# Performance work log

Hardware: AMD Instinct MI355X
Metric: run time of the kernel (lower is better)

## Reference

```python
import jax, jax.numpy as jnp
import numpy as np

B, S, H, D, DM = 2, 512, 8, 32, 256  # batch, seq_len, n_head, d_k, d_model


def setup_inputs() -> dict:
    key = jax.random.key(0)
    ks = jax.random.split(key, 8)
    scale = 0.02
    return {
        "hidden_states": jax.random.normal(ks[0], (B, S, DM), dtype=jnp.float32),
        "rpe": jax.random.normal(ks[1], (B, S, S, D), dtype=jnp.float32),
        "w_q": jax.random.normal(ks[2], (DM, H * D), dtype=jnp.float32) * scale,
        "w_k": jax.random.normal(ks[3], (DM, H * D), dtype=jnp.float32) * scale,
        "w_v": jax.random.normal(ks[4], (DM, H * D), dtype=jnp.float32) * scale,
        "fc_w": jax.random.normal(ks[5], (H * D, DM), dtype=jnp.float32) * scale,
        "fc_b": jnp.zeros((DM,), dtype=jnp.float32),
        "ln_w": jnp.ones((DM,), dtype=jnp.float32),
        "ln_b": jnp.zeros((DM,), dtype=jnp.float32),
        "station_num": 256,
    }


def reference(hidden_states, rpe, w_q, w_k, w_v, fc_w, fc_b, ln_w, ln_b, station_num):
    b, s, dm = hidden_states.shape
    d = rpe.shape[-1]
    h = w_q.shape[1] // d

    def heads(x, w):
        # (b, s, dm) @ (dm, h*d) -> (b, h, s, d)
        return (x @ w).reshape(b, s, h, d).transpose(0, 2, 1, 3)

    q = heads(hidden_states, w_q)
    k = heads(hidden_states, w_k)
    v = heads(hidden_states, w_v)

    # torch: (q.unsqueeze(2) * k.unsqueeze(3) * rpe.unsqueeze(1)).sum(-1)
    # scores[b,h,i,j] = sum_d q[b,h,j,d] * k[b,h,i,d] * rpe[b,i,j,d]
    scores = jnp.einsum('bhjd,bhid,bijd->bhij', q, k, rpe) / jnp.sqrt(jnp.float32(d))

    # shielded mask: column j visible if j < station_num, plus the diagonal
    col = jnp.arange(s) < station_num                  # (s,)
    mask = col[None, :] | jnp.eye(s, dtype=bool)        # (s, s)
    scores = jnp.where(mask[None, None], scores, jnp.float32(-1e10))

    attn = jax.nn.softmax(scores, axis=-1)              # (b, h, s, s)
    out = jnp.einsum('bhij,bhjd->bhid', attn, v)        # (b, h, s, d)
    out = out.transpose(0, 2, 1, 3).reshape(b, s, h * d)

    ctx = out @ fc_w + fc_b + hidden_states             # residual
    mu = jnp.mean(ctx, axis=-1, keepdims=True)
    var = jnp.mean(jnp.square(ctx - mu), axis=-1, keepdims=True)
    ctx = (ctx - mu) / jnp.sqrt(var + 1e-6) * ln_w + ln_b
    return ctx
```

## Files before the change

kernel.cpp:

```cpp
#include <hip/hip_runtime.h>
#include <hip/hip_bf16.h>

#define B_  2
#define S_  512
#define H_  8
#define D_  32
#define DM_ 256
#define HD_ 256
#define NROW 4
#define TI  2
#define HC  2
#define NR  (TI * HC)

__global__ __launch_bounds__(256) void qkv_kernel(
    const float* __restrict__ hid, const float* __restrict__ wq,
    const float* __restrict__ wk, const float* __restrict__ wv,
    float* __restrict__ qo, float* __restrict__ ko, float* __restrict__ vo)
{
  __shared__ float hs[NROW][DM_];
  const int r0 = blockIdx.x * NROW;
  const float* w   = (blockIdx.y == 0) ? wq : (blockIdx.y == 1) ? wk : wv;
  float*       out = (blockIdx.y == 0) ? qo : (blockIdx.y == 1) ? ko : vo;
  const float mulf = (blockIdx.y == 0) ? 0.17677669529663687f : 1.0f;
  const int tid = threadIdx.x;

  for (int idx = tid; idx < NROW * DM_; idx += 256)
    hs[idx >> 8][idx & 255] = hid[r0 * DM_ + idx];
  __syncthreads();

  float acc[NROW] = {0.f, 0.f, 0.f, 0.f};
  const float* wp = w + tid;
  #pragma unroll 8
  for (int c4 = 0; c4 < DM_ / 4; ++c4) {
    const float w0 = wp[(4 * c4 + 0) * HD_];
    const float w1 = wp[(4 * c4 + 1) * HD_];
    const float w2 = wp[(4 * c4 + 2) * HD_];
    const float w3 = wp[(4 * c4 + 3) * HD_];
    #pragma unroll
    for (int r = 0; r < NROW; ++r) {
      const float4 hv = reinterpret_cast<const float4*>(&hs[r][0])[c4];
      acc[r] = fmaf(hv.x, w0, acc[r]);
      acc[r] = fmaf(hv.y, w1, acc[r]);
      acc[r] = fmaf(hv.z, w2, acc[r]);
      acc[r] = fmaf(hv.w, w3, acc[r]);
    }
  }
  const int h = tid >> 5, d = tid & 31;
  #pragma unroll
  for (int r = 0; r < NROW; ++r) {
    const int g = r0 + r;
    const int b = g >> 9, s = g & (S_ - 1);
    out[((b * H_ + h) * S_ + s) * D_ + d] = acc[r] * mulf;
  }
}

__device__ __forceinline__ float red4(float x) {
  int i;
  i = __builtin_amdgcn_mov_dpp(__float_as_int(x), 0xB1, 0xf, 0xf, true);
  x += __int_as_float(i);
  i = __builtin_amdgcn_mov_dpp(__float_as_int(x), 0x4E, 0xf, 0xf, true);
  x += __int_as_float(i);
  return x;
}

__global__ __launch_bounds__(256, 4) void attn_kernel(
    const float* __restrict__ rpe, const float* __restrict__ q_ws,
    const float* __restrict__ k_ws, const float* __restrict__ v_ws,
    const int* __restrict__ station_p, float* __restrict__ o_ws)
{
  __shared__ float p_smem[NR * S_];
  __shared__ float sums[NR];

  const int tid  = threadIdx.x;
  const int w    = tid >> 6, lane = tid & 63;
  const int j4   = lane >> 2, dq = lane & 3;
  const int j8   = lane >> 3, dc = lane & 7;
  const int n    = blockIdx.x;
  const int hg   = (n >> 3) & 3;
  const int t    = (n & 7) | ((n >> 5) << 3);
  const int b    = t >> 8;
  const int i0   = (t & 255) * TI;
  const int h0   = hg * HC;
  const int HS   = S_ * D_;

  int station = station_p[0];
  station = station > S_ ? S_ : (station < 0 ? 0 : station);

  const float* qb = q_ws + (size_t)((b * H_ + h0) * S_) * D_;
  const float* kb = k_ws + (size_t)((b * H_ + h0) * S_ + i0) * D_;
  const float* vb = v_ws + (size_t)((b * H_ + h0) * S_) * D_;
  const float* rb = rpe + ((size_t)b * S_ + i0) * S_ * D_;

  float4 kf[HC][TI][2];
  #pragma unroll
  for (int hh = 0; hh < HC; ++hh)
    #pragma unroll
    for (int ii = 0; ii < TI; ++ii) {
      kf[hh][ii][0] = *reinterpret_cast<const float4*>(kb + hh * HS + ii * D_ + dq * 8);
      kf[hh][ii][1] = *reinterpret_cast<const float4*>(kb + hh * HS + ii * D_ + dq * 8 + 4);
    }

  for (int jb = w * 16; jb < station; jb += 64) {
    const int j  = jb + j4;
    const int jc = j < S_ ? j : S_ - 1;
    float4 q[HC][2];
    #pragma unroll
    for (int hh = 0; hh < HC; ++hh) {
      q[hh][0] = *reinterpret_cast<const float4*>(qb + hh * HS + jc * D_ + dq * 8);
      q[hh][1] = *reinterpret_cast<const float4*>(qb + hh * HS + jc * D_ + dq * 8 + 4);
    }
    float4 rv[TI][2];
    #pragma unroll
    for (int ii = 0; ii < TI; ++ii) {
      rv[ii][0] = *reinterpret_cast<const float4*>(rb + ii * HS + jc * D_ + dq * 8);
      rv[ii][1] = *reinterpret_cast<const float4*>(rb + ii * HS + jc * D_ + dq * 8 + 4);
    }
    #pragma unroll
    for (int hh = 0; hh < HC; ++hh)
      #pragma unroll
      for (int ii = 0; ii < TI; ++ii) {
        float s = q[hh][0].x * kf[hh][ii][0].x * rv[ii][0].x;
        s = fmaf(q[hh][0].y * kf[hh][ii][0].y, rv[ii][0].y, s);
        s = fmaf(q[hh][0].z * kf[hh][ii][0].z, rv[ii][0].z, s);
        s = fmaf(q[hh][0].w * kf[hh][ii][0].w, rv[ii][0].w, s);
        s = fmaf(q[hh][1].x * kf[hh][ii][1].x, rv[ii][1].x, s);
        s = fmaf(q[hh][1].y * kf[hh][ii][1].y, rv[ii][1].y, s);
        s = fmaf(q[hh][1].z * kf[hh][ii][1].z, rv[ii][1].z, s);
        s = fmaf(q[hh][1].w * kf[hh][ii][1].w, rv[ii][1].w, s);
        s = red4(s);
        if (dq == 0 && j < station) p_smem[(hh * TI + ii) * S_ + j] = s;
      }
  }
  if (w == 0 && j4 < TI) {
    const int j = i0 + j4;
    if (j >= station) {
      const float4 r0 = *reinterpret_cast<const float4*>(rb + j4 * HS + j * D_ + dq * 8);
      const float4 r1 = *reinterpret_cast<const float4*>(rb + j4 * HS + j * D_ + dq * 8 + 4);
      #pragma unroll
      for (int hh = 0; hh < HC; ++hh) {
        const float4 q0 = *reinterpret_cast<const float4*>(qb + hh * HS + j * D_ + dq * 8);
        const float4 q1 = *reinterpret_cast<const float4*>(qb + hh * HS + j * D_ + dq * 8 + 4);
        const float4 k0 = *reinterpret_cast<const float4*>(kb + hh * HS + j4 * D_ + dq * 8);
        const float4 k1 = *reinterpret_cast<const float4*>(kb + hh * HS + j4 * D_ + dq * 8 + 4);
        float s = q0.x * k0.x * r0.x;
        s = fmaf(q0.y * k0.y, r0.y, s);
        s = fmaf(q0.z * k0.z, r0.z, s);
        s = fmaf(q0.w * k0.w, r0.w, s);
        s = fmaf(q1.x * k1.x, r1.x, s);
        s = fmaf(q1.y * k1.y, r1.y, s);
        s = fmaf(q1.z * k1.z, r1.z, s);
        s = fmaf(q1.w * k1.w, r1.w, s);
        s = red4(s);
        if (dq == 0) p_smem[(hh * TI + j4) * S_ + j] = s;
      }
    }
  }
  __syncthreads();

  {
    const int r  = w;
    const int ii = r & (TI - 1);
    const int ig = i0 + ii;
    const bool dx = (ig >= station);
    float m = -1e30f;
    for (int jj = lane; jj < station; jj += 64) m = fmaxf(m, p_smem[r * S_ + jj]);
    const float dv = dx ? p_smem[r * S_ + ig] : -1e30f;
    m = fmaxf(m, dv);
    #pragma unroll
    for (int o = 32; o; o >>= 1) m = fmaxf(m, __shfl_xor(m, o, 64));
    float sum = 0.f;
    for (int jj = lane; jj < station; jj += 64) {
      const float e = __expf(p_smem[r * S_ + jj] - m);
      p_smem[r * S_ + jj] = e;
      sum += e;
    }
    #pragma unroll
    for (int o = 32; o; o >>= 1) sum += __shfl_xor(sum, o, 64);
    if (dx) {
      const float e = __expf(dv - m);
      sum += e;
      if (lane == 0) p_smem[r * S_ + ig] = e;
    }
    if (lane == 0) sums[r] = sum;
  }
  __syncthreads();

  float4 acc[HC][TI];
  #pragma unroll
  for (int hh = 0; hh < HC; ++hh)
    #pragma unroll
    for (int ii = 0; ii < TI; ++ii) acc[hh][ii] = make_float4(0.f, 0.f, 0.f, 0.f);

  for (int jb = w * 8; jb < station; jb += 32) {
    const int j  = jb + j8;
    const int jc = j < S_ ? j : S_ - 1;
    float4 v4[HC];
    #pragma unroll
    for (int hh = 0; hh < HC; ++hh)
      v4[hh] = *reinterpret_cast<const float4*>(vb + hh * HS + jc * D_ + dc * 4);
    #pragma unroll
    for (int hh = 0; hh < HC; ++hh)
      #pragma unroll
      for (int ii = 0; ii < TI; ++ii) {
        float pv = 0.f;
        if (j < station) pv = p_smem[(hh * TI + ii) * S_ + j];
        acc[hh][ii].x = fmaf(pv, v4[hh].x, acc[hh][ii].x);
        acc[hh][ii].y = fmaf(pv, v4[hh].y, acc[hh][ii].y);
        acc[hh][ii].z = fmaf(pv, v4[hh].z, acc[hh][ii].z);
        acc[hh][ii].w = fmaf(pv, v4[hh].w, acc[hh][ii].w);
      }
  }
  if (w == 0 && j8 == 0) {
    #pragma unroll
    for (int ii = 0; ii < TI; ++ii) {
      const int ig = i0 + ii;
      if (ig >= station) {
        #pragma unroll
        for (int hh = 0; hh < HC; ++hh) {
          const float pv = p_smem[(hh * TI + ii) * S_ + ig];
          const float4 v4 = *reinterpret_cast<const float4*>(vb + hh * HS + ig * D_ + dc * 4);
          acc[hh][ii].x = fmaf(pv, v4.x, acc[hh][ii].x);
          acc[hh][ii].y = fmaf(pv, v4.y, acc[hh][ii].y);
          acc[hh][ii].z = fmaf(pv, v4.z, acc[hh][ii].z);
          acc[hh][ii].w = fmaf(pv, v4.w, acc[hh][ii].w);
        }
      }
    }
  }
  __syncthreads();

  float4* redv = reinterpret_cast<float4*>(p_smem);
  #pragma unroll
  for (int hh = 0; hh < HC; ++hh)
    #pragma unroll
    for (int ii = 0; ii < TI; ++ii) {
      const int r = hh * TI + ii;
      float4 a = acc[hh][ii];
      a.x += __shfl_xor(a.x, 8);
      a.y += __shfl_xor(a.y, 8);
      a.z += __shfl_xor(a.z, 8);
      a.w += __shfl_xor(a.w, 8);
      if ((j8 & 1) == 0)
        redv[((w * 4 + (j8 >> 1)) * NR + r) * 8 + dc] = a;
    }
  __syncthreads();
  if (tid < NR * 8) {
    const int r = tid >> 3, d4 = tid & 7;
    float4 a = make_float4(0.f, 0.f, 0.f, 0.f);
    #pragma unroll
    for (int g = 0; g < 16; ++g) {
      const float4 x = redv[(g * NR + r) * 8 + d4];
      a.x += x.x; a.y += x.y; a.z += x.z; a.w += x.w;
    }
    const float inv = 1.f / sums[r];
    a.x *= inv; a.y *= inv; a.z *= inv; a.w *= inv;
    const int hh = r >> 1, ii = r & 1;
    reinterpret_cast<float4*>(
        o_ws + (size_t)((b * H_ + h0 + hh) * S_ + i0 + ii) * D_)[d4] = a;
  }
}

__global__ __launch_bounds__(256) void fc_ln_kernel(
    const float* __restrict__ o_ws, const float* __restrict__ fc_w,
    const float* __restrict__ fc_b, const float* __restrict__ hid,
    const float* __restrict__ ln_w, const float* __restrict__ ln_b,
    float* __restrict__ out)
{
  __shared__ float orow[NROW][HD_];
  __shared__ float red[NROW][4];
  const int tid = threadIdx.x;
  const int r0 = blockIdx.x * NROW;

  for (int idx = tid; idx < NROW * HD_; idx += 256) {
    const int r = idx >> 8, m = idx & 255;
    const int g = r0 + r;
    const int b = g >> 9, i = g & (S_ - 1);
    orow[r][m] = o_ws[((b * H_ + (m >> 5)) * S_ + i) * D_ + (m & 31)];
  }
  __syncthreads();

  float acc[NROW] = {0.f, 0.f, 0.f, 0.f};
  const float* wp = fc_w + tid;
  #pragma unroll 8
  for (int n4 = 0; n4 < HD_ / 4; ++n4) {
    const float w0 = wp[(4 * n4 + 0) * DM_];
    const float w1 = wp[(4 * n4 + 1) * DM_];
    const float w2 = wp[(4 * n4 + 2) * DM_];
    const float w3 = wp[(4 * n4 + 3) * DM_];
    #pragma unroll
    for (int r = 0; r < NROW; ++r) {
      const float4 ov = reinterpret_cast<const float4*>(&orow[r][0])[n4];
      acc[r] = fmaf(ov.x, w0, acc[r]);
      acc[r] = fmaf(ov.y, w1, acc[r]);
      acc[r] = fmaf(ov.z, w2, acc[r]);
      acc[r] = fmaf(ov.w, w3, acc[r]);
    }
  }
  const float bias = fc_b[tid];
  #pragma unroll
  for (int r = 0; r < NROW; ++r) acc[r] += bias + hid[(r0 + r) * DM_ + tid];

  const int w = tid >> 6, lane = tid & 63;
  float mu[NROW];
  #pragma unroll
  for (int r = 0; r < NROW; ++r) {
    float s = acc[r];
    #pragma unroll
    for (int o = 32; o; o >>= 1) s += __shfl_xor(s, o, 64);
    if (lane == 0) red[r][w] = s;
  }
  __syncthreads();
  #pragma unroll
  for (int r = 0; r < NROW; ++r)
    mu[r] = (red[r][0] + red[r][1] + red[r][2] + red[r][3]) * (1.f / DM_);
  __syncthreads();
  #pragma unroll
  for (int r = 0; r < NROW; ++r) {
    const float dd = acc[r] - mu[r];
    float s = dd * dd;
    #pragma unroll
    for (int o = 32; o; o >>= 1) s += __shfl_xor(s, o, 64);
    if (lane == 0) red[r][w] = s;
  }
  __syncthreads();
  const float lw = ln_w[tid], lb = ln_b[tid];
  #pragma unroll
  for (int r = 0; r < NROW; ++r) {
    const float var = (red[r][0] + red[r][1] + red[r][2] + red[r][3]) * (1.f / DM_);
    out[(r0 + r) * DM_ + tid] =
        (acc[r] - mu[r]) * rsqrtf(var + 1e-6f) * lw + lb;
  }
}

extern "C" void kernel_launch(void* const* d_in, const int* in_sizes, int n_in,
                              void* d_out, int out_size, void* d_ws, size_t ws_size,
                              hipStream_t stream) {
  const float* hid = (const float*)d_in[0];
  const float* rpe = (const float*)d_in[1];
  const float* wq  = (const float*)d_in[2];
  const float* wk  = (const float*)d_in[3];
  const float* wv  = (const float*)d_in[4];
  const float* fcw = (const float*)d_in[5];
  const float* fcb = (const float*)d_in[6];
  const float* lnw = (const float*)d_in[7];
  const float* lnb = (const float*)d_in[8];
  const int* station = (const int*)d_in[9];
  float* out = (float*)d_out;

  const size_t per = (size_t)B_ * H_ * S_ * D_;
  float* q_ws = (float*)d_ws;
  float* k_ws = q_ws + per;
  float* v_ws = k_ws + per;
  float* o_ws = v_ws + per;

  dim3 gA(B_ * S_ / NROW, 3);
  qkv_kernel<<<gA, 256, 0, stream>>>(hid, wq, wk, wv, q_ws, k_ws, v_ws);
  attn_kernel<<<B_ * (S_ / TI) * (H_ / HC), 256, 0, stream>>>(
      rpe, q_ws, k_ws, v_ws, station, o_ws);
  fc_ln_kernel<<<B_ * S_ / NROW, 256, 0, stream>>>(o_ws, fcw, fcb, hid, lnw, lnb, out);
}
```

Before: 156.7 us.

## Stream rpe tiles into double-buffered LDS via global_load_lds DMA

```diff
diff --git a/kernel.cpp b/kernel.cpp
--- a/kernel.cpp
+++ b/kernel.cpp
@@ -11,6 +11,7 @@
 #define TI  2
 #define HC  2
 #define NR  (TI * HC)
+#define JC  32
 
 __global__ __launch_bounds__(256) void qkv_kernel(
     const float* __restrict__ hid, const float* __restrict__ wq,
@@ -54,27 +55,38 @@
   }
 }
 
-__device__ __forceinline__ float red4(float x) {
+__device__ __forceinline__ float red8(float x) {
   int i;
   i = __builtin_amdgcn_mov_dpp(__float_as_int(x), 0xB1, 0xf, 0xf, true);
   x += __int_as_float(i);
   i = __builtin_amdgcn_mov_dpp(__float_as_int(x), 0x4E, 0xf, 0xf, true);
   x += __int_as_float(i);
+  i = __builtin_amdgcn_mov_dpp(__float_as_int(x), 0x124, 0xf, 0xf, true);
+  x += __int_as_float(i);
   return x;
 }
 
-__global__ __launch_bounds__(256, 4) void attn_kernel(
+__device__ __forceinline__ void lds_dma16(float* dst_uniform, const float* src) {
+  __builtin_amdgcn_global_load_lds(
+      (const __attribute__((address_space(1))) unsigned int*)src,
+      (__attribute__((address_space(3))) unsigned int*)dst_uniform,
+      16, 0, 0);
+}
+
+__global__ __launch_bounds__(256, 6) void attn_kernel(
     const float* __restrict__ rpe, const float* __restrict__ q_ws,
     const float* __restrict__ k_ws, const float* __restrict__ v_ws,
     const int* __restrict__ station_p, float* __restrict__ o_ws)
 {
-  __shared__ float p_smem[NR * S_];
+  __shared__ __align__(16) float rpe_smem[2][TI * JC * D_];
+  __shared__ __align__(16) float p_smem[NR * S_];
   __shared__ float sums[NR];
 
   const int tid  = threadIdx.x;
   const int w    = tid >> 6, lane = tid & 63;
-  const int j4   = lane >> 2, dq = lane & 3;
-  const int j8   = lane >> 3, dc = lane & 7;
+  const int jl   = tid >> 3;
+  const int dc   = tid & 7;
+  const int j8   = lane >> 3;
   const int n    = blockIdx.x;
   const int hg   = (n >> 3) & 3;
   const int t    = (n & 7) | ((n >> 5) << 3);
@@ -85,73 +97,100 @@
 
   int station = station_p[0];
   station = station > S_ ? S_ : (station < 0 ? 0 : station);
+  const int NC = (station + JC - 1) / JC;
 
   const float* qb = q_ws + (size_t)((b * H_ + h0) * S_) * D_;
   const float* kb = k_ws + (size_t)((b * H_ + h0) * S_ + i0) * D_;
   const float* vb = v_ws + (size_t)((b * H_ + h0) * S_) * D_;
   const float* rb = rpe + ((size_t)b * S_ + i0) * S_ * D_;
 
-  float4 kf[HC][TI][2];
+  float4 kf[HC][TI];
   #pragma unroll
   for (int hh = 0; hh < HC; ++hh)
     #pragma unroll
-    for (int ii = 0; ii < TI; ++ii) {
-      kf[hh][ii][0] = *reinterpret_cast<const float4*>(kb + hh * HS + ii * D_ + dq * 8);
-      kf[hh][ii][1] = *reinterpret_cast<const float4*>(kb + hh * HS + ii * D_ + dq * 8 + 4);
-    }
-
-  for (int jb = w * 16; jb < station; jb += 64) {
-    const int j  = jb + j4;
-    const int jc = j < S_ ? j : S_ - 1;
-    float4 q[HC][2];
-    #pragma unroll
-    for (int hh = 0; hh < HC; ++hh) {
-      q[hh][0] = *reinterpret_cast<const float4*>(qb + hh * HS + jc * D_ + dq * 8);
-      q[hh][1] = *reinterpret_cast<const float4*>(qb + hh * HS + jc * D_ + dq * 8 + 4);
-    }
-    float4 rv[TI][2];
-    #pragma unroll
-    for (int ii = 0; ii < TI; ++ii) {
-      rv[ii][0] = *reinterpret_cast<const float4*>(rb + ii * HS + jc * D_ + dq * 8);
-      rv[ii][1] = *reinterpret_cast<const float4*>(rb + ii * HS + jc * D_ + dq * 8 + 4);
-    }
-    #pragma unroll
-    for (int hh = 0; hh < HC; ++hh)
+    for (int ii = 0; ii < TI; ++ii)
+      kf[hh][ii] = *reinterpret_cast<const float4*>(kb + hh * HS + ii * D_ + dc * 4);
+
+  if (NC > 0) {
+    #pragma unroll
+    for (int it = 0; it < 2; ++it) {
+      const int m = w * 2 + it;
+      const float* src = rb + (m >> 2) * HS
+                       + (size_t)(((m & 3) * 8) + (lane >> 3)) * D_ + (lane & 7) * 4;
+      lds_dma16(&rpe_smem[0][m * 256], src);
+    }
+  }
+  __syncthreads();
+
+  for (int c = 0; c < NC; ++c) {
+    if (c + 1 < NC) {
+      const int jb = (c + 1) * JC;
       #pragma unroll
-      for (int ii = 0; ii < TI; ++ii) {
-        float s = q[hh][0].x * kf[hh][ii][0].x * rv[ii][0].x;
-        s = fmaf(q[hh][0].y * kf[hh][ii][0].y, rv[ii][0].y, s);
-        s = fmaf(q[hh][0].z * kf[hh][ii][0].z, rv[ii][0].z, s);
-        s = fmaf(q[hh][0].w * kf[hh][ii][0].w, rv[ii][0].w, s);
-        s = fmaf(q[hh][1].x * kf[hh][ii][1].x, rv[ii][1].x, s);
-        s = fmaf(q[hh][1].y * kf[hh][ii][1].y, rv[ii][1].y, s);
-        s = fmaf(q[hh][1].z * kf[hh][ii][1].z, rv[ii][1].z, s);
-        s = fmaf(q[hh][1].w * kf[hh][ii][1].w, rv[ii][1].w, s);
-        s = red4(s);
-        if (dq == 0 && j < station) p_smem[(hh * TI + ii) * S_ + j] = s;
+      for (int it = 0; it < 2; ++it) {
+        const int m = w * 2 + it;
+        const float* src = rb + (m >> 2) * HS
+                         + (size_t)(jb + ((m & 3) * 8) + (lane >> 3)) * D_ + (lane & 7) * 4;
+        lds_dma16(&rpe_smem[(c + 1) & 1][m * 256], src);
       }
-  }
-  if (w == 0 && j4 < TI) {
-    const int j = i0 + j4;
+    }
+    const float* buf = rpe_smem[c & 1];
+    const int j = c * JC + jl;
+    const float4 rv0 = *reinterpret_cast<const float4*>(buf + tid * 4);
+    const float4 rv1 = *reinterpret_cast<const float4*>(buf + (256 + tid) * 4);
+    const float4 q0 = *reinterpret_cast<const float4*>(qb + (size_t)j * D_ + dc * 4);
+    const float4 q1 = *reinterpret_cast<const float4*>(qb + HS + (size_t)j * D_ + dc * 4);
+    const bool st = (dc == 0) && (j < station);
+
+    float s;
+    s = q0.x * kf[0][0].x * rv0.x;
+    s = fmaf(q0.y * kf[0][0].y, rv0.y, s);
+    s = fmaf(q0.z * kf[0][0].z, rv0.z, s);
+    s = fmaf(q0.w * kf[0][0].w, rv0.w, s);
+    s = red8(s);
+    if (st) p_smem[0 * S_ + j] = s;
+
+    s = q0.x * kf[0][1].x * rv1.x;
+    s = fmaf(q0.y * kf[0][1].y, rv1.y, s);
+    s = fmaf(q0.z * kf[0][1].z, rv1.z, s);
+    s = fmaf(q0.w * kf[0][1].w, rv1.w, s);
+    s = red8(s);
+    if (st) p_smem[1 * S_ + j] = s;
+
+    s = q1.x * kf[1][0].x * rv0.x;
+    s = fmaf(q1.y * kf[1][0].y, rv0.y, s);
+    s = fmaf(q1.z * kf[1][0].z, rv0.z, s);
+    s = fmaf(q1.w * kf[1][0].w, rv0.w, s);
+    s = red8(s);
+    if (st) p_smem[2 * S_ + j] = s;
+
+    s = q1.x * kf[1][1].x * rv1.x;
+    s = fmaf(q1.y * kf[1][1].y, rv1.y, s);
+    s = fmaf(q1.z * kf[1][1].z, rv1.z, s);
+    s = fmaf(q1.w * kf[1][1].w, rv1.w, s);
+    s = red8(s);
+    if (st) p_smem[3 * S_ + j] = s;
+
+    __syncthreads();
+  }
+
+  if (w == 0 && lane < TI * 8) {
+    const int ii = lane >> 3;
+    const int j = i0 + ii;
     if (j >= station) {
-      const float4 r0 = *reinterpret_cast<const float4*>(rb + j4 * HS + j * D_ + dq * 8);
-      const float4 r1 = *reinterpret_cast<const float4*>(rb + j4 * HS + j * D_ + dq * 8 + 4);
+      const float4 rv = *reinterpret_cast<const float4*>(
+          rb + ii * HS + (size_t)j * D_ + dc * 4);
       #pragma unroll
       for (int hh = 0; hh < HC; ++hh) {
-        const float4 q0 = *reinterpret_cast<const float4*>(qb + hh * HS + j * D_ + dq * 8);
-        const float4 q1 = *reinterpret_cast<const float4*>(qb + hh * HS + j * D_ + dq * 8 + 4);
-        const float4 k0 = *reinterpret_cast<const float4*>(kb + hh * HS + j4 * D_ + dq * 8);
-        const float4 k1 = *reinterpret_cast<const float4*>(kb + hh * HS + j4 * D_ + dq * 8 + 4);
-        float s = q0.x * k0.x * r0.x;
-        s = fmaf(q0.y * k0.y, r0.y, s);
-        s = fmaf(q0.z * k0.z, r0.z, s);
-        s = fmaf(q0.w * k0.w, r0.w, s);
-        s = fmaf(q1.x * k1.x, r1.x, s);
-        s = fmaf(q1.y * k1.y, r1.y, s);
-        s = fmaf(q1.z * k1.z, r1.z, s);
-        s = fmaf(q1.w * k1.w, r1.w, s);
-        s = red4(s);
-        if (dq == 0) p_smem[(hh * TI + j4) * S_ + j] = s;
+        const float4 q4 = *reinterpret_cast<const float4*>(
+            qb + hh * HS + (size_t)j * D_ + dc * 4);
+        const float4 k4 = *reinterpret_cast<const float4*>(
+            kb + hh * HS + ii * D_ + dc * 4);
+        float s = q4.x * k4.x * rv.x;
+        s = fmaf(q4.y * k4.y, rv.y, s);
+        s = fmaf(q4.z * k4.z, rv.z, s);
+        s = fmaf(q4.w * k4.w, rv.w, s);
+        s = red8(s);
+        if (dc == 0) p_smem[(hh * TI + ii) * S_ + j] = s;
       }
     }
   }
```

Result: no change. 159.5 us (+1.8%).
